# Optimization experiments

Measured on AMD Instinct MI355X. Metric: run time of the kernel, lower is better.

Reference implementation:

```python
import jax, jax.numpy as jnp
import numpy as np

N_CLASSES = 8  # hardcoded by the (-1, 8, 8) reshape in the original layer

def setup_inputs() -> dict:
    key = jax.random.key(0)
    k1, k2, k3, k4 = jax.random.split(key, 4)
    B, F, C, R = 16384, 128, N_CLASSES, 64
    x = jax.random.normal(k1, (B, F), dtype=jnp.float32)
    p = jax.random.uniform(k2, (B, C), dtype=jnp.float32)  # class-prob-like input
    W = jax.random.normal(k3, (F, C * C, R), dtype=jnp.float32) * 0.02
    b = jax.random.normal(k4, (C, C, R), dtype=jnp.float32) * 0.1
    return {"x": x, "p": p, "W": W, "b": b}

def reference(x, p, W, b):
    # x: (B, 128) features; p: (B, C) class probs; W: (128, C*C, R); b: (C, C, R)
    B = x.shape[0]
    C = b.shape[0]
    R = b.shape[-1]
    # per-annotator GEMM fused across all annotators: (B, C*C, R)
    logits = jnp.einsum('bf,fkr->bkr', x, W).reshape(B, C, C, R) + b[None]
    # row-softmax: softmax over the "predicted class" axis for each true class c
    M = jax.nn.softmax(logits, axis=2)  # (B, C, C, R)
    # batched dot: p (B,C) contracted against rows of each annotator matrix
    out = jnp.einsum('bc,bcdr->bdr', p, M)  # (B, C, R)
    # NOTE: original applies K.dropout(0.5) (training-mode); omitted for a
    # deterministic inference reference (identity at eval).
    return out
```

## Files before the change

kernel.cpp:

```cpp
#include <hip/hip_runtime.h>
#include <hip/hip_bf16.h>


#define F_DIM    128
#define NCOL     4096
#define OUT_STRIDE 512
#define LOG2E    1.44269504088896340736f

typedef __bf16 bf16x8 __attribute__((ext_vector_type(8)));
typedef float  f32x4  __attribute__((ext_vector_type(4)));
typedef float  f32x16 __attribute__((ext_vector_type(16)));

#define AS1(p) ((const __attribute__((address_space(1))) unsigned int*)(p))
#define AS3(p) ((__attribute__((address_space(3))) unsigned int*)(p))

__global__ void wconv_kernel(const float* __restrict__ W,
                             const float* __restrict__ p,
                             const float* __restrict__ bias,
                             __bf16* __restrict__ wf,
                             float* __restrict__ pT,
                             float* __restrict__ bias_r) {
    int f    = blockIdx.x * 256 + threadIdx.x;
    int lane = f & 63;
    int gf   = f >> 6;
    int kst  = gf & 7;
    int w4   = (gf >> 3) & 15;
    int c    = gf >> 7;
    int m    = lane & 31;
    int kbase = kst * 16 + (lane >> 5) * 8;
    int n     = c * 512 + (m & 7) * 64 + w4 * 4 + (m >> 3);
    bf16x8 frag;
#pragma unroll
    for (int j = 0; j < 8; ++j)
        frag[j] = (__bf16)(W[(kbase + j) * NCOL + n] * LOG2E);
    *(bf16x8*)(wf + (size_t)f * 8) = frag;

#pragma unroll
    for (int u = f; u < 131072; u += 65536)
        pT[u] = p[(size_t)(u & 16383) * 8 + (u >> 14)];

    if (f < 4096) {
        int cc = f >> 9, ww4 = (f >> 5) & 15, mm = f & 31;
        bias_r[f] = bias[cc * 512 + (mm & 7) * 64 + ww4 * 4 + (mm >> 3)] * LOG2E;
    }
}

__global__ __launch_bounds__(256, 5)
void fused_kernel(const float* __restrict__ x, const float* __restrict__ pT,
                  const float* __restrict__ bias_r, const __bf16* __restrict__ wf,
                  float* __restrict__ out) {
    __shared__ __align__(16) char lds[16384];

    const int lane = threadIdx.x & 63;
    const int ww   = threadIdx.x >> 6;
    const int l31  = lane & 31;
    const int h    = lane >> 5;
    const int w4   = blockIdx.x >> 7;
    const int g    = blockIdx.x & 127;
    const int b0w  = g * 128 + ww * 32;

#pragma unroll
    for (int s = 0; s < 2; ++s) {
        int kst = ww * 2 + s;
        int gfr = w4 * 8 + kst;
        __builtin_amdgcn_global_load_lds(
            AS1((const char*)wf + (size_t)gfr * 1024 + lane * 16),
            AS3(lds + kst * 1024), 16, 0, 0);
    }

    bf16x8 xfr[8];
    {
        const float* xr = x + (size_t)(b0w + l31) * F_DIM + h * 8;
#pragma unroll
        for (int kst = 0; kst < 8; ++kst) {
            float4 lo = *(const float4*)(xr + kst * 16);
            float4 hi = *(const float4*)(xr + kst * 16 + 4);
            bf16x8 fr;
            fr[0] = (__bf16)lo.x; fr[1] = (__bf16)lo.y;
            fr[2] = (__bf16)lo.z; fr[3] = (__bf16)lo.w;
            fr[4] = (__bf16)hi.x; fr[5] = (__bf16)hi.y;
            fr[6] = (__bf16)hi.z; fr[7] = (__bf16)hi.w;
            xfr[kst] = fr;
        }
    }

    float O[16] = {};

#pragma unroll 1
    for (int c = 0; c < 8; ++c) {
        __syncthreads();

        if (c < 7) {
            char* dst = lds + ((c + 1) & 1) * 8192;
#pragma unroll
            for (int s = 0; s < 2; ++s) {
                int kst = ww * 2 + s;
                int gfr = ((c + 1) * 16 + w4) * 8 + kst;
                __builtin_amdgcn_global_load_lds(
                    AS1((const char*)wf + (size_t)gfr * 1024 + lane * 16),
                    AS3(dst + kst * 1024), 16, 0, 0);
            }
        }

        float pv = pT[(size_t)c * 16384 + b0w + l31];

        f32x4 bvl[4];
#pragma unroll
        for (int r2 = 0; r2 < 4; ++r2)
            bvl[r2] = *(const f32x4*)(bias_r + (c * 16 + w4) * 32 + r2 * 8 + h * 4);

        f32x16 acc;
#pragma unroll
        for (int i = 0; i < 16; ++i)
            acc[i] = bvl[i >> 2][i & 3];

        const char* buf = lds + (c & 1) * 8192;
#pragma unroll
        for (int kst = 0; kst < 8; ++kst) {
            bf16x8 af = *(const bf16x8*)(buf + kst * 1024 + lane * 16);
            acc = __builtin_amdgcn_mfma_f32_32x32x16_bf16(af, xfr[kst], acc, 0, 0, 0);
        }

#pragma unroll
        for (int r2 = 0; r2 < 4; ++r2) {
            float e0 = __builtin_amdgcn_exp2f(acc[r2 * 4 + 0]);
            float e1 = __builtin_amdgcn_exp2f(acc[r2 * 4 + 1]);
            float e2 = __builtin_amdgcn_exp2f(acc[r2 * 4 + 2]);
            float e3 = __builtin_amdgcn_exp2f(acc[r2 * 4 + 3]);
            float s4 = (e0 + e1) + (e2 + e3);
            float s8 = s4 + __shfl_xor(s4, 32, 64);
            float scale = pv * __builtin_amdgcn_rcpf(s8);
            O[r2 * 4 + 0] = __builtin_fmaf(e0, scale, O[r2 * 4 + 0]);
            O[r2 * 4 + 1] = __builtin_fmaf(e1, scale, O[r2 * 4 + 1]);
            O[r2 * 4 + 2] = __builtin_fmaf(e2, scale, O[r2 * 4 + 2]);
            O[r2 * 4 + 3] = __builtin_fmaf(e3, scale, O[r2 * 4 + 3]);
        }
    }

#pragma unroll
    for (int q = 0; q < 4; ++q) {
        f32x4 v = {O[q], O[4 + q], O[8 + q], O[12 + q]};
        *(f32x4*)(out + (size_t)(b0w + l31) * OUT_STRIDE + (q + 4 * h) * 64 + w4 * 4) = v;
    }
}

extern "C" void kernel_launch(void* const* d_in, const int* in_sizes, int n_in,
                              void* d_out, int out_size, void* d_ws, size_t ws_size,
                              hipStream_t stream) {
    const float* x    = (const float*)d_in[0];
    const float* p    = (const float*)d_in[1];
    const float* W    = (const float*)d_in[2];
    const float* bias = (const float*)d_in[3];
    float* out = (float*)d_out;
    __bf16* wf     = (__bf16*)d_ws;
    float*  pT     = (float*)((char*)d_ws + (1 << 20));
    float*  bias_r = (float*)((char*)d_ws + (1 << 20) + (512 << 10));

    wconv_kernel<<<dim3(256), dim3(256), 0, stream>>>(W, p, bias, wf, pT, bias_r);
    fused_kernel<<<dim3(2048), dim3(256), 0, stream>>>(x, pT, bias_r, wf, out);
}
```

Baseline: 114.3 us.

## Retile fused kernel to 512-thread blocks with LDS-staged coalesced output writes

Each block now covers 64 batch rows and 4 adjacent annotator groups (16 R-columns), using 8 waves in place of 4 and a 64KB LDS double buffer for the weight fragments. At the end, results are transposed through LDS so every output row gets a contiguous 64-byte write instead of scattered 16-byte stores. The goal is to coalesce the output stores, which are the dominant memory traffic. In exchange, the larger LDS footprint and block size lower occupancy, and x is reloaded per block across fewer batch rows.

```diff
diff --git a/kernel.cpp b/kernel.cpp
--- a/kernel.cpp
+++ b/kernel.cpp
@@ -45,32 +45,35 @@
     }
 }
 
-__global__ __launch_bounds__(256, 5)
+__global__ __launch_bounds__(512, 4)
 void fused_kernel(const float* __restrict__ x, const float* __restrict__ pT,
                   const float* __restrict__ bias_r, const __bf16* __restrict__ wf,
                   float* __restrict__ out) {
-    __shared__ __align__(16) char lds[16384];
+    __shared__ __align__(16) char lds[65536];
 
     const int lane = threadIdx.x & 63;
     const int ww   = threadIdx.x >> 6;
+    const int bg   = ww >> 2;
+    const int w4s  = ww & 3;
     const int l31  = lane & 31;
     const int h    = lane >> 5;
-    const int w4   = blockIdx.x >> 7;
-    const int g    = blockIdx.x & 127;
-    const int b0w  = g * 128 + ww * 32;
+    const int w16  = blockIdx.x >> 8;
+    const int g    = blockIdx.x & 255;
+    const int b0   = g * 64 + bg * 32;
+    const int w4   = w16 * 4 + w4s;
 
 #pragma unroll
-    for (int s = 0; s < 2; ++s) {
-        int kst = ww * 2 + s;
+    for (int s = 0; s < 4; ++s) {
+        int kst = bg * 4 + s;
         int gfr = w4 * 8 + kst;
         __builtin_amdgcn_global_load_lds(
             AS1((const char*)wf + (size_t)gfr * 1024 + lane * 16),
-            AS3(lds + kst * 1024), 16, 0, 0);
+            AS3(lds + (w4s * 8 + kst) * 1024), 16, 0, 0);
     }
 
     bf16x8 xfr[8];
     {
-        const float* xr = x + (size_t)(b0w + l31) * F_DIM + h * 8;
+        const float* xr = x + (size_t)(b0 + l31) * F_DIM + h * 8;
 #pragma unroll
         for (int kst = 0; kst < 8; ++kst) {
             float4 lo = *(const float4*)(xr + kst * 16);
@@ -91,18 +94,18 @@
         __syncthreads();
 
         if (c < 7) {
-            char* dst = lds + ((c + 1) & 1) * 8192;
+            char* dst = lds + ((c + 1) & 1) * 32768;
 #pragma unroll
-            for (int s = 0; s < 2; ++s) {
-                int kst = ww * 2 + s;
+            for (int s = 0; s < 4; ++s) {
+                int kst = bg * 4 + s;
                 int gfr = ((c + 1) * 16 + w4) * 8 + kst;
                 __builtin_amdgcn_global_load_lds(
                     AS1((const char*)wf + (size_t)gfr * 1024 + lane * 16),
-                    AS3(dst + kst * 1024), 16, 0, 0);
+                    AS3(dst + (w4s * 8 + kst) * 1024), 16, 0, 0);
             }
         }
 
-        float pv = pT[(size_t)c * 16384 + b0w + l31];
+        float pv = pT[(size_t)c * 16384 + b0 + l31];
 
         f32x4 bvl[4];
 #pragma unroll
@@ -114,10 +117,10 @@
         for (int i = 0; i < 16; ++i)
             acc[i] = bvl[i >> 2][i & 3];
 
-        const char* buf = lds + (c & 1) * 8192;
+        const char* buf = lds + (c & 1) * 32768;
 #pragma unroll
         for (int kst = 0; kst < 8; ++kst) {
-            bf16x8 af = *(const bf16x8*)(buf + kst * 1024 + lane * 16);
+            bf16x8 af = *(const bf16x8*)(buf + (w4s * 8 + kst) * 1024 + lane * 16);
             acc = __builtin_amdgcn_mfma_f32_32x32x16_bf16(af, xfr[kst], acc, 0, 0, 0);
         }
 
@@ -137,10 +140,28 @@
         }
     }
 
+    __syncthreads();
+
+    float* L = (float*)lds;
 #pragma unroll
-    for (int q = 0; q < 4; ++q) {
-        f32x4 v = {O[q], O[4 + q], O[8 + q], O[12 + q]};
-        *(f32x4*)(out + (size_t)(b0w + l31) * OUT_STRIDE + (q + 4 * h) * 64 + w4 * 4) = v;
+    for (int i = 0; i < 16; ++i) {
+        int d    = (i & 3) + 4 * h;
+        int rloc = w4s * 4 + (i >> 2);
+        L[(d * 16 + rloc) * 66 + bg * 32 + l31] = O[i];
+    }
+    __syncthreads();
+
+#pragma unroll
+    for (int j = 0; j < 4; ++j) {
+        int linear = threadIdx.x * 4 + j * 2048;
+        int bq = linear >> 7;
+        int dr = linear & 127;
+        f32x4 v;
+#pragma unroll
+        for (int k = 0; k < 4; ++k)
+            v[k] = L[(dr + k) * 66 + bq];
+        *(f32x4*)(out + (size_t)(g * 64 + bq) * OUT_STRIDE
+                      + (dr >> 4) * 64 + w16 * 16 + (dr & 15)) = v;
     }
 }
 
@@ -157,5 +178,5 @@
     float*  bias_r = (float*)((char*)d_ws + (1 << 20) + (512 << 10));
 
     wconv_kernel<<<dim3(256), dim3(256), 0, stream>>>(W, p, bias, wf, pT, bias_r);
-    fused_kernel<<<dim3(2048), dim3(256), 0, stream>>>(x, pT, bias_r, wf, out);
+    fused_kernel<<<dim3(1024), dim3(512), 0, stream>>>(x, pT, bias_r, wf, out);
 }
```

Result: slower. 118.2 us (+3.4%).
